# Performance work log

Measured on AMD Instinct MI355X. Metric: run time of the kernel, lower is better.

Reference implementation:

```python
import jax, jax.numpy as jnp
import numpy as np

B, DIM, H, W = 32, 256, 64, 64
WIN, SHIFT, HEADS = 8, 4, 8
HEAD_DIM = DIM // HEADS
SCALE = HEAD_DIM ** -0.5
N = WIN * WIN


def _window_partition(x, ws):
    # x: (B, H, W, C) -> (B*nW, ws, ws, C)
    b, h, w, c = x.shape
    x = x.reshape(b, h // ws, ws, w // ws, ws, c)
    return x.transpose(0, 1, 3, 2, 4, 5).reshape(-1, ws, ws, c)


def _window_reverse(windows, ws, h, w):
    # windows: (B*nW, ws, ws, C) -> (B, H, W, C)
    b = windows.shape[0] // ((h // ws) * (w // ws))
    x = windows.reshape(b, h // ws, w // ws, ws, ws, -1)
    return x.transpose(0, 1, 3, 2, 4, 5).reshape(b, h, w, -1)


def _rel_pos_index(ws):
    coords = np.stack(np.meshgrid(np.arange(ws), np.arange(ws), indexing='ij'))  # (2,ws,ws)
    cf = coords.reshape(2, -1)
    rel = cf[:, :, None] - cf[:, None, :]  # (2,N,N)
    rel = rel.transpose(1, 2, 0)
    rel[:, :, 0] += ws - 1
    rel[:, :, 1] += ws - 1
    rel[:, :, 0] *= 2 * ws - 1
    return rel.sum(-1)  # (N,N) int


def _shift_mask(h, w, ws, shift):
    img_mask = np.zeros((1, h, w, 1), np.float32)
    slices = (slice(0, -ws), slice(-ws, -shift), slice(-shift, None))
    cnt = 0
    for hs in slices:
        for wsl in slices:
            img_mask[:, hs, wsl, :] = cnt
            cnt += 1
    mw = np.asarray(_window_partition(jnp.asarray(img_mask), ws)).reshape(-1, ws * ws)
    am = mw[:, None, :] - mw[:, :, None]  # (nW, N, N)
    return jnp.asarray(np.where(am != 0, -100.0, 0.0).astype(np.float32))


_REL_IDX = jnp.asarray(_rel_pos_index(WIN).reshape(-1))  # (N*N,)
_ATTN_MASK = _shift_mask(H, W, WIN, SHIFT)  # (nW, N, N)


def setup_inputs() -> dict:
    key = jax.random.key(0)
    k1, k2, k3, k4 = jax.random.split(key, 4)
    x = jax.random.normal(k1, (B, DIM, H, W), jnp.float32)
    qkv_w = jax.random.normal(k2, (DIM, 3 * DIM), jnp.float32) * (DIM ** -0.5)
    qkv_b = jax.random.normal(k3, (3 * DIM,), jnp.float32) * 0.02
    rel_bias_table = jax.random.normal(k4, ((2 * WIN - 1) ** 2, HEADS), jnp.float32) * 0.02
    return {"x": x, "qkv_w": qkv_w, "qkv_b": qkv_b, "rel_bias_table": rel_bias_table}


def reference(x, qkv_w, qkv_b, rel_bias_table):
    b, c, h, w = x.shape
    xp = x.transpose(0, 2, 3, 1)  # (B,H,W,C)
    xs = jnp.roll(xp, (-SHIFT, -SHIFT), axis=(1, 2))
    win = _window_partition(xs, WIN).reshape(-1, N, c)  # (BW,N,C)
    bw = win.shape[0]
    qkv = win @ qkv_w + qkv_b  # (BW,N,3C)
    qkv = qkv.reshape(bw, N, 3, HEADS, HEAD_DIM).transpose(2, 0, 3, 1, 4)
    q, k, v = qkv[0], qkv[1], qkv[2]  # (BW,heads,N,hd)
    attn = jnp.einsum('whnd,whmd->whnm', q * SCALE, k)  # (BW,heads,N,N)
    bias = rel_bias_table[_REL_IDX].reshape(N, N, HEADS).transpose(2, 0, 1)  # (heads,N,N)
    attn = attn + bias[None]
    n_win = _ATTN_MASK.shape[0]
    attn = attn.reshape(b, n_win, HEADS, N, N) + _ATTN_MASK[None, :, None]
    attn = jax.nn.softmax(attn.reshape(bw, HEADS, N, N), axis=-1)
    out = jnp.einsum('whnm,whmd->whnd', attn, v)  # (BW,heads,N,hd)
    out = out.transpose(0, 2, 1, 3).reshape(bw, N, DIM)
    out = out.reshape(-1, WIN, WIN, DIM)
    out = _window_reverse(out, WIN, h, w)  # (B,H,W,C)
    out = jnp.roll(out, (SHIFT, SHIFT), axis=(1, 2))
    return out.transpose(0, 3, 1, 2)  # (B,C,H,W)
```

## Files before the change

### kernel.cpp

```cpp
#include <hip/hip_runtime.h>


typedef __attribute__((ext_vector_type(8))) short short8;
typedef __attribute__((ext_vector_type(4))) float f32x4;

static __device__ __forceinline__ short f2bf(float f) {
    unsigned u = __float_as_uint(f);
    u = (u + 0x7fffu + ((u >> 16) & 1u)) >> 16;
    return (short)u;
}

static __device__ __forceinline__ int region(int i) {
    return (i < 56) ? 0 : ((i < 60) ? 1 : 2);
}

static __device__ __forceinline__ void barrier_lds() {
    asm volatile("s_waitcnt lgkmcnt(0)" ::: "memory");
    __builtin_amdgcn_s_barrier();
    asm volatile("" ::: "memory");
}

static __device__ __forceinline__ float dpp_max16(float x) {
    float t;
    t = __int_as_float(__builtin_amdgcn_update_dpp(__float_as_int(x), __float_as_int(x), 0xB1, 0xF, 0xF, true));
    x = fmaxf(x, t);
    t = __int_as_float(__builtin_amdgcn_update_dpp(__float_as_int(x), __float_as_int(x), 0x4E, 0xF, 0xF, true));
    x = fmaxf(x, t);
    t = __int_as_float(__builtin_amdgcn_update_dpp(__float_as_int(x), __float_as_int(x), 0x141, 0xF, 0xF, true));
    x = fmaxf(x, t);
    t = __int_as_float(__builtin_amdgcn_update_dpp(__float_as_int(x), __float_as_int(x), 0x140, 0xF, 0xF, true));
    x = fmaxf(x, t);
    return x;
}

static __device__ __forceinline__ float dpp_sum16(float x) {
    float t;
    t = __int_as_float(__builtin_amdgcn_update_dpp(__float_as_int(x), __float_as_int(x), 0xB1, 0xF, 0xF, true));
    x += t;
    t = __int_as_float(__builtin_amdgcn_update_dpp(__float_as_int(x), __float_as_int(x), 0x4E, 0xF, 0xF, true));
    x += t;
    t = __int_as_float(__builtin_amdgcn_update_dpp(__float_as_int(x), __float_as_int(x), 0x141, 0xF, 0xF, true));
    x += t;
    t = __int_as_float(__builtin_amdgcn_update_dpp(__float_as_int(x), __float_as_int(x), 0x140, 0xF, 0xF, true));
    x += t;
    return x;
}

__global__ void wt_transpose(const float* __restrict__ w, unsigned short* __restrict__ wt) {
    int col = blockIdx.x;
    int k   = threadIdx.x;
    float v = w[k * 768 + col];
    unsigned u = __float_as_uint(v);
    u = (u + 0x7fffu + ((u >> 16) & 1u)) >> 16;
    wt[col * 256 + k] = (unsigned short)u;
}

__global__ __launch_bounds__(512, 4) void swin_kernel(
    const float* __restrict__ x,
    const unsigned short* __restrict__ wt,
    const float* __restrict__ qkv_b,
    const float* __restrict__ tbl,
    float* __restrict__ out)
{
    __shared__ char smem[80384];
    unsigned short* w_s = (unsigned short*)(smem);

    const int tid  = threadIdx.x;
    const int wave = tid >> 6;
    const int lane = tid & 63;
    const int ln   = lane & 15;
    const int quad = lane >> 4;
    const int win  = wave >> 2;
    const int wv   = wave & 3;

    const int blk = blockIdx.x;
    const int b   = blk >> 5;
    const int wh  = (blk >> 2) & 7;
    const int wp  = blk & 3;
    const int ww  = wp * 2 + win;

    unsigned short* q_s  = (unsigned short*)(smem + 50688 + win * 14848);
    unsigned short* k_s  = (unsigned short*)(smem + 50688 + win * 14848 + 5120);
    unsigned short* vt_s = (unsigned short*)(smem + 50688 + win * 14848 + 10240);
    unsigned short* p_s  = (unsigned short*)(smem + win * 17664);
    float*          o_s  = (float*)(smem + win * 17664 + 9216);

    const int t_a  = wv * 16 + ln;
    const int ti_a = t_a >> 3, tj_a = t_a & 7;
    const int si = (wh * 8 + ti_a + 4) & 63;
    const int sj = (ww * 8 + tj_a + 4) & 63;
    const float* xb = x + ((size_t)b * 256) * 4096 + si * 64 + sj;
    short8 afrag[8];
    #pragma unroll
    for (int ks = 0; ks < 8; ++ks) {
        #pragma unroll
        for (int j = 0; j < 8; ++j) {
            int c = ks * 32 + quad * 8 + j;
            afrag[ks][j] = f2bf(xb[(size_t)c * 4096]);
        }
    }

    const int row0 = wv * 16 + quad * 4;

    unsigned mmask = 0;
    unsigned idxp[4];
    #pragma unroll
    for (int nt = 0; nt < 4; ++nt) {
        int tk = nt * 16 + ln;
        int tik = tk >> 3, tjk = tk & 7;
        int cntk = region(wh * 8 + tik) * 3 + region(ww * 8 + tjk);
        unsigned pk = 0;
        #pragma unroll
        for (int r = 0; r < 4; ++r) {
            int tq = row0 + r;
            int tiq = tq >> 3, tjq = tq & 7;
            int idx = (tiq - tik + 7) * 15 + (tjq - tjk + 7);
            pk |= (unsigned)idx << (8 * r);
            int cntq = region(wh * 8 + tiq) * 3 + region(ww * 8 + tjq);
            if (cntq != cntk) mmask |= 1u << (nt * 4 + r);
        }
        idxp[nt] = pk;
    }

    for (int h = 0; h < 8; ++h) {
        barrier_lds();

        #pragma unroll
        for (int i = 0; i < 6; ++i) {
            int idx = i * 512 + tid;
            int cl  = idx >> 5;
            int ch  = idx & 31;
            int col = ((cl >> 5) << 8) + (h << 5) + (cl & 31);
            short8 wv8 = *(const short8*)(wt + col * 256 + ch * 8);
            *(short8*)(w_s + cl * 264 + ch * 8) = wv8;
        }
        barrier_lds();

        f32x4 acc[6];
        #pragma unroll
        for (int jt = 0; jt < 6; ++jt) acc[jt] = (f32x4){0.f, 0.f, 0.f, 0.f};
        #pragma unroll
        for (int ks = 0; ks < 8; ++ks) {
            short8 a = afrag[ks];
            #pragma unroll
            for (int jt = 0; jt < 6; ++jt) {
                short8 bb = *(const short8*)(w_s + (jt * 16 + ln) * 264 + ks * 32 + quad * 8);
                acc[jt] = __builtin_amdgcn_mfma_f32_16x16x32_bf16(a, bb, acc[jt], 0, 0, 0);
            }
        }
        #pragma unroll
        for (int jt = 0; jt < 6; ++jt) {
            int colL = jt * 16 + ln;
            int seg  = colL >> 5;
            int cc   = colL & 31;
            float bias = qkv_b[(seg << 8) + (h << 5) + cc];
            #pragma unroll
            for (int r = 0; r < 4; ++r) {
                float v = acc[jt][r] + bias;
                int tok = row0 + r;
                if (seg == 0)      q_s[tok * 40 + cc] = (unsigned short)f2bf(v * 0.17677669529663689f);
                else if (seg == 1) k_s[tok * 40 + cc] = (unsigned short)f2bf(v);
                else               vt_s[cc * 72 + tok] = (unsigned short)f2bf(v);
            }
        }
        barrier_lds();

        short8 aq = *(const short8*)(q_s + (wv * 16 + ln) * 40 + quad * 8);
        f32x4 sacc[4];
        #pragma unroll
        for (int nt = 0; nt < 4; ++nt) {
            short8 bk = *(const short8*)(k_s + (nt * 16 + ln) * 40 + quad * 8);
            f32x4 z = (f32x4){0.f, 0.f, 0.f, 0.f};
            sacc[nt] = __builtin_amdgcn_mfma_f32_16x16x32_bf16(aq, bk, z, 0, 0, 0);
        }
        float sv[4][4];
        #pragma unroll
        for (int nt = 0; nt < 4; ++nt) {
            #pragma unroll
            for (int r = 0; r < 4; ++r) {
                int idx = (idxp[nt] >> (8 * r)) & 255;
                float s = sacc[nt][r] + tbl[idx * 8 + h];
                s += ((mmask >> (nt * 4 + r)) & 1) ? -100.0f : 0.0f;
                sv[nt][r] = s;
            }
        }
        #pragma unroll
        for (int r = 0; r < 4; ++r) {
            float m = fmaxf(fmaxf(sv[0][r], sv[1][r]), fmaxf(sv[2][r], sv[3][r]));
            m = dpp_max16(m);
            float p0 = __expf(sv[0][r] - m);
            float p1 = __expf(sv[1][r] - m);
            float p2 = __expf(sv[2][r] - m);
            float p3 = __expf(sv[3][r] - m);
            float ssum = dpp_sum16(p0 + p1 + p2 + p3);
            float inv = __builtin_amdgcn_rcpf(ssum);
            int pr = (row0 + r) * 72;
            p_s[pr +      ln] = (unsigned short)f2bf(p0 * inv);
            p_s[pr + 16 + ln] = (unsigned short)f2bf(p1 * inv);
            p_s[pr + 32 + ln] = (unsigned short)f2bf(p2 * inv);
            p_s[pr + 48 + ln] = (unsigned short)f2bf(p3 * inv);
        }

        f32x4 oacc[2];
        oacc[0] = (f32x4){0.f, 0.f, 0.f, 0.f};
        oacc[1] = (f32x4){0.f, 0.f, 0.f, 0.f};
        #pragma unroll
        for (int ks = 0; ks < 2; ++ks) {
            short8 ap = *(const short8*)(p_s + (wv * 16 + ln) * 72 + ks * 32 + quad * 8);
            #pragma unroll
            for (int nt = 0; nt < 2; ++nt) {
                short8 bv = *(const short8*)(vt_s + (nt * 16 + ln) * 72 + ks * 32 + quad * 8);
                oacc[nt] = __builtin_amdgcn_mfma_f32_16x16x32_bf16(ap, bv, oacc[nt], 0, 0, 0);
            }
        }
        #pragma unroll
        for (int nt = 0; nt < 2; ++nt)
            #pragma unroll
            for (int r = 0; r < 4; ++r)
                o_s[(row0 + r) * 33 + nt * 16 + ln] = oacc[nt][r];
        barrier_lds();

        {
            int tl  = tid & 255;
            int cl  = tl & 31;
            int ti2 = tl >> 5;
            f32x4 v0, v1;
            #pragma unroll
            for (int tj = 0; tj < 4; ++tj) v0[tj] = o_s[(ti2 * 8 + tj) * 33 + cl];
            #pragma unroll
            for (int tj = 0; tj < 4; ++tj) v1[tj] = o_s[(ti2 * 8 + 4 + tj) * 33 + cl];
            int c  = (h << 5) + cl;
            int di = (wh * 8 + ti2 + 4) & 63;
            float* op = out + ((size_t)(b * 256 + c)) * 4096 + di * 64;
            *(f32x4*)(op + (ww * 8 + 4))        = v0;
            *(f32x4*)(op + ((ww * 8 + 8) & 63)) = v1;
        }
    }
}

extern "C" void kernel_launch(void* const* d_in, const int* in_sizes, int n_in,
                              void* d_out, int out_size, void* d_ws, size_t ws_size,
                              hipStream_t stream) {
    const float* x      = (const float*)d_in[0];
    const float* qkv_w  = (const float*)d_in[1];
    const float* qkv_b  = (const float*)d_in[2];
    const float* tbl    = (const float*)d_in[3];
    float* out          = (float*)d_out;
    unsigned short* Wt  = (unsigned short*)d_ws;

    wt_transpose<<<dim3(768), dim3(256), 0, stream>>>(qkv_w, Wt);
    swin_kernel<<<dim3(1024), dim3(512), 0, stream>>>(x, Wt, qkv_b, tbl, out);
}
```

Baseline: 502.2 us.

## Prefetch next head's weights into registers, tile weight transpose, use nontemporal stores

The per-head weight slice is now loaded from global memory into registers one head ahead, during the QKV MFMA loop, so the latency overlaps compute instead of sitting between barriers. The weight transpose kernel becomes an LDS-tiled transpose with coalesced reads and writes. Output writes use nontemporal stores to reduce cache pollution. The prefetch adds 24 VGPRs per thread, which could pressure the fixed 4-waves-per-EU occupancy target.

Result: slower. 588.8 us (+17.3%).

```diff
diff --git a/kernel.cpp b/kernel.cpp
--- a/kernel.cpp
+++ b/kernel.cpp
@@ -46,16 +46,29 @@
     return x;
 }
 
-__global__ void wt_transpose(const float* __restrict__ w, unsigned short* __restrict__ wt) {
-    int col = blockIdx.x;
-    int k   = threadIdx.x;
-    float v = w[k * 768 + col];
-    unsigned u = __float_as_uint(v);
-    u = (u + 0x7fffu + ((u >> 16) & 1u)) >> 16;
-    wt[col * 256 + k] = (unsigned short)u;
-}
-
-__global__ __launch_bounds__(512, 4) void swin_kernel(
+__global__ __launch_bounds__(256) void wt_transpose(const float* __restrict__ w,
+                                                    unsigned short* __restrict__ wt) {
+    __shared__ unsigned short t[64][72];
+    int bx = blockIdx.x;
+    int by = blockIdx.y;
+    int tx = threadIdx.x & 63;
+    int ty = threadIdx.x >> 6;
+    #pragma unroll
+    for (int i = 0; i < 16; ++i) {
+        int k = i * 4 + ty;
+        t[k][tx] = (unsigned short)f2bf(w[(by * 64 + k) * 768 + bx * 64 + tx]);
+    }
+    __syncthreads();
+    #pragma unroll
+    for (int i = 0; i < 16; ++i) {
+        int c = i * 4 + ty;
+        wt[(size_t)(bx * 64 + c) * 256 + by * 64 + tx] = t[tx][c];
+    }
+}
+
+__global__ __launch_bounds__(512)
+__attribute__((amdgpu_waves_per_eu(4, 4)))
+void swin_kernel(
     const float* __restrict__ x,
     const unsigned short* __restrict__ wt,
     const float* __restrict__ qkv_b,
@@ -122,6 +135,16 @@
         idxp[nt] = pk;
     }
 
+    short8 wpre[6];
+    #pragma unroll
+    for (int i = 0; i < 6; ++i) {
+        int idx = i * 512 + tid;
+        int cl  = idx >> 5;
+        int ch  = idx & 31;
+        int col = ((cl >> 5) << 8) + (cl & 31);
+        wpre[i] = *(const short8*)(wt + col * 256 + ch * 8);
+    }
+
     for (int h = 0; h < 8; ++h) {
         barrier_lds();
 
@@ -130,9 +153,7 @@
             int idx = i * 512 + tid;
             int cl  = idx >> 5;
             int ch  = idx & 31;
-            int col = ((cl >> 5) << 8) + (h << 5) + (cl & 31);
-            short8 wv8 = *(const short8*)(wt + col * 256 + ch * 8);
-            *(short8*)(w_s + cl * 264 + ch * 8) = wv8;
+            *(short8*)(w_s + cl * 264 + ch * 8) = wpre[i];
         }
         barrier_lds();
 
@@ -148,6 +169,18 @@
                 acc[jt] = __builtin_amdgcn_mfma_f32_16x16x32_bf16(a, bb, acc[jt], 0, 0, 0);
             }
         }
+
+        if (h < 7) {
+            #pragma unroll
+            for (int i = 0; i < 6; ++i) {
+                int idx = i * 512 + tid;
+                int cl  = idx >> 5;
+                int ch  = idx & 31;
+                int col = ((cl >> 5) << 8) + ((h + 1) << 5) + (cl & 31);
+                wpre[i] = *(const short8*)(wt + col * 256 + ch * 8);
+            }
+        }
+
         #pragma unroll
         for (int jt = 0; jt < 6; ++jt) {
             int colL = jt * 16 + ln;
@@ -232,8 +265,8 @@
             int c  = (h << 5) + cl;
             int di = (wh * 8 + ti2 + 4) & 63;
             float* op = out + ((size_t)(b * 256 + c)) * 4096 + di * 64;
-            *(f32x4*)(op + (ww * 8 + 4))        = v0;
-            *(f32x4*)(op + ((ww * 8 + 8) & 63)) = v1;
+            __builtin_nontemporal_store(v0, (f32x4*)(op + (ww * 8 + 4)));
+            __builtin_nontemporal_store(v1, (f32x4*)(op + ((ww * 8 + 8) & 63)));
         }
     }
 }
@@ -248,6 +281,6 @@
     float* out          = (float*)d_out;
     unsigned short* Wt  = (unsigned short*)d_ws;
 
-    wt_transpose<<<dim3(768), dim3(256), 0, stream>>>(qkv_w, Wt);
+    wt_transpose<<<dim3(12, 4), dim3(256), 0, stream>>>(qkv_w, Wt);
     swin_kernel<<<dim3(1024), dim3(512), 0, stream>>>(x, Wt, qkv_b, tbl, out);
 }
```
